# Optimization experiments

Hardware: AMD Instinct MI355X
Metric: run time of the kernel (lower is better)

## Reference

```python
import jax, jax.numpy as jnp
import numpy as np
import math

C_MUL = 32            # multiplicity per irrep
N_NODES = 20000
N_EDGES = 320000
N_RBF = 16
# CG-allowed paths (l_in, l_sh, l_out) with l_in in {0,1}, l_sh,l_out in {0,1,2}
PATHS = [(0,0,0),(0,1,1),(0,2,2),(1,0,1),(1,1,0),(1,1,1),(1,1,2),(1,2,1),(1,2,2)]
DIM_IN = C_MUL * 4
DIM_OUT = C_MUL * 9
N_W = len(PATHS) * C_MUL


def _cg_complex(l1, l2, l3):
    """Clebsch-Gordan coefficients in the complex SH basis (Racah formula)."""
    f = math.factorial
    C = np.zeros((2*l1+1, 2*l2+1, 2*l3+1))
    for m1 in range(-l1, l1+1):
        for m2 in range(-l2, l2+1):
            m3 = m1 + m2
            if abs(m3) > l3:
                continue
            pref = math.sqrt((2*l3+1) * f(l1+l2-l3) * f(l1-l2+l3) * f(-l1+l2+l3) / f(l1+l2+l3+1))
            pref *= math.sqrt(f(l3+m3) * f(l3-m3) * f(l1-m1) * f(l1+m1) * f(l2-m2) * f(l2+m2))
            s = 0.0
            for k in range(0, l1+l2-l3+1):
                args = [k, l1+l2-l3-k, l1-m1-k, l2+m2-k, l3-l2+m1+k, l3-l1-m2+k]
                if min(args) < 0:
                    continue
                d = 1.0
                for a in args:
                    d *= f(a)
                s += (-1.0)**k / d
            C[m1+l1, m2+l2, m3+l3] = pref * s
    return C


def _u_real(l):
    """Complex->real SH change of basis, rows indexed by real m=-l..l."""
    U = np.zeros((2*l+1, 2*l+1), dtype=complex)
    U[l, l] = 1.0
    s = 1.0 / math.sqrt(2.0)
    for m in range(1, l+1):
        U[l+m, l+m] = (-1)**m * s
        U[l+m, l-m] = s
        U[l-m, l-m] = 1j * s
        U[l-m, l+m] = -1j * (-1)**m * s
    return U


def _cg_real(l1, l2, l3):
    """CG coefficients in the real SH basis (real up to a global phase)."""
    Cc = _cg_complex(l1, l2, l3).astype(complex)
    T = np.einsum('am,bn,co,mno->abc', _u_real(l1), _u_real(l2), np.conj(_u_real(l3)), Cc)
    R = T.real if np.abs(T.real).max() >= np.abs(T.imag).max() else T.imag
    return np.ascontiguousarray(R).astype(np.float32)

CGS = [jnp.asarray(_cg_real(*p)) for p in PATHS]


def _sph(v):
    """Real spherical harmonics (l=0,1,2) of unit vectors v: list of (E,1),(E,3),(E,5)."""
    x, y, z = v[:, 0], v[:, 1], v[:, 2]
    s3 = math.sqrt(3.0)
    y0 = jnp.ones_like(x)[:, None]
    y1 = jnp.stack([y, z, x], axis=-1)                       # m = -1, 0, 1
    y2 = jnp.stack([s3*x*y, s3*y*z, 0.5*(3.0*z*z - 1.0), s3*x*z, 0.5*s3*(x*x - y*y)], axis=-1)
    return [y0, y1, y2]


def _tfn_forward(node_features, edge_features, edge_vectors, edge_index, W0, W1, W2):
    E = edge_index.shape[0]
    N = node_features.shape[0]
    # normalized edge vectors -> spherical harmonic basis
    v = edge_vectors / (jnp.linalg.norm(edge_vectors, axis=-1, keepdims=True) + 1e-12)
    Y = _sph(v)
    # radial filter network: Dense->swish x3, bias-free (activation after last layer too)
    h = jax.nn.silu(edge_features @ W0)
    h = jax.nn.silu(h @ W1)
    w = jax.nn.silu(h @ W2)                                  # (E, 9*C)
    # gather source node features and split into irrep blocks
    src = node_features[edge_index[:, 0]]                    # (E, 128)
    xin = [src[:, :C_MUL].reshape(E, C_MUL, 1),              # l=0 block
           src[:, C_MUL:].reshape(E, C_MUL, 3)]              # l=1 block
    outs = [jnp.zeros((E, C_MUL, 2*l+1), node_features.dtype) for l in (0, 1, 2)]
    for p, (l1, l2, l3) in enumerate(PATHS):
        wp = w[:, p*C_MUL:(p+1)*C_MUL]                       # (E, C) per-channel path weight
        contrib = jnp.einsum('abc,eua,eb->euc', CGS[p], xin[l1], Y[l2])
        outs[l3] = outs[l3] + contrib * wp[:, :, None]
    msg = jnp.concatenate([o.reshape(E, -1) for o in outs], axis=-1)   # (E, 288)
    # scatter-add messages to destination nodes
    return jax.ops.segment_sum(msg, edge_index[:, 1], num_segments=N)


def setup_inputs() -> dict:
    key = jax.random.key(0)
    ks = jax.random.split(key, 7)
    node_features = jax.random.normal(ks[0], (N_NODES, DIM_IN), jnp.float32)
    edge_features = jax.random.uniform(ks[1], (N_EDGES, N_RBF), jnp.float32)
    edge_vectors = jax.random.normal(ks[2], (N_EDGES, 3), jnp.float32)
    edge_index = jax.random.randint(ks[3], (N_EDGES, 2), 0, N_NODES, dtype=jnp.int32)
    W0 = jax.random.normal(ks[4], (N_RBF, 64), jnp.float32) * math.sqrt(2.0 / N_RBF)
    W1 = jax.random.normal(ks[5], (64, 64), jnp.float32) * math.sqrt(2.0 / 64)
    W2 = jax.random.normal(ks[6], (64, N_W), jnp.float32) * math.sqrt(2.0 / 64)
    return {"node_features": node_features, "edge_features": edge_features,
            "edge_vectors": edge_vectors, "edge_index": edge_index,
            "W0": W0, "W1": W1, "W2": W2}


def reference(node_features, edge_features, edge_vectors, edge_index, W0, W1, W2):
    return _tfn_forward(node_features, edge_features, edge_vectors, edge_index, W0, W1, W2)
```

## Files before the change

kernel.cpp:

```cpp
#include <hip/hip_runtime.h>
#include <hip/hip_bf16.h>
#include <math.h>

#define TPB 256
#define TE  64
#define HP  72
#define EP  40
#define WP  72
#define CP  90
#define QC  80

#define WBF_USH 26624

typedef float  v4f __attribute__((ext_vector_type(4)));
typedef short  s8v __attribute__((ext_vector_type(8)));
typedef float  f4v __attribute__((ext_vector_type(4)));


__device__ double dfact(int n){ double r = 1.0; for (int i = 2; i <= n; ++i) r *= (double)i; return r; }

__device__ void build_u(int l, double ur[5][5], double ui[5][5]){
  for (int i = 0; i < 5; ++i) for (int j = 0; j < 5; ++j){ ur[i][j] = 0.0; ui[i][j] = 0.0; }
  ur[l][l] = 1.0;
  double s = 1.0 / sqrt(2.0);
  for (int m = 1; m <= l; ++m){
    double sg = (m & 1) ? -1.0 : 1.0;
    ur[l + m][l + m] = sg * s;
    ur[l + m][l - m] = s;
    ui[l - m][l - m] = s;
    ui[l - m][l + m] = -sg * s;
  }
}

__device__ void cg_compute(int tid, float* __restrict__ cg){
  if (tid >= 245) return;
  const int L1[9]  = {0,0,0,1,1,1,1,1,1};
  const int L2[9]  = {0,1,2,0,1,1,1,2,2};
  const int L3[9]  = {0,1,2,1,0,1,2,1,2};
  const int OFF[10] = {0,1,10,35,44,53,80,125,170,245};
  int p = 0;
  while (p < 8 && tid >= OFF[p+1]) ++p;
  int idx = tid - OFF[p];
  int l1 = L1[p], l2 = L2[p], l3 = L3[p];
  int n1 = 2*l1+1, n2 = 2*l2+1, n3 = 2*l3+1;
  int c = idx % n3; int ab = idx / n3; int b = ab % n2; int a = ab / n2;

  double Cc[5][5][5];
  for (int i = 0; i < 5; ++i) for (int j = 0; j < 5; ++j) for (int k = 0; k < 5; ++k) Cc[i][j][k] = 0.0;
  for (int m1 = -l1; m1 <= l1; ++m1) for (int m2 = -l2; m2 <= l2; ++m2){
    int m3 = m1 + m2;
    if (m3 < -l3 || m3 > l3) continue;
    double pref = sqrt((double)(2*l3+1) * dfact(l1+l2-l3) * dfact(l1-l2+l3) * dfact(-l1+l2+l3) / dfact(l1+l2+l3+1));
    pref *= sqrt(dfact(l3+m3)*dfact(l3-m3)*dfact(l1-m1)*dfact(l1+m1)*dfact(l2-m2)*dfact(l2+m2));
    double s = 0.0;
    for (int k = 0; k <= l1 + l2 - l3; ++k){
      int a0 = k, a1 = l1+l2-l3-k, a2 = l1-m1-k, a3 = l2+m2-k, a4 = l3-l2+m1+k, a5 = l3-l1-m2+k;
      if (a0 < 0 || a1 < 0 || a2 < 0 || a3 < 0 || a4 < 0 || a5 < 0) continue;
      double dd = dfact(a0)*dfact(a1)*dfact(a2)*dfact(a3)*dfact(a4)*dfact(a5);
      s += ((k & 1) ? -1.0 : 1.0) / dd;
    }
    Cc[m1+l1][m2+l2][m3+l3] = pref * s;
  }

  double U1r[5][5], U1i[5][5], U2r[5][5], U2i[5][5], U3r[5][5], U3i[5][5];
  build_u(l1, U1r, U1i); build_u(l2, U2r, U2i); build_u(l3, U3r, U3i);

  double sr = 0.0, si = 0.0;
  for (int m = 0; m < n1; ++m) for (int n = 0; n < n2; ++n) for (int o = 0; o < n3; ++o){
    double cc = Cc[m][n][o];
    if (cc == 0.0) continue;
    double xre = U1r[a][m], xim = U1i[a][m];
    double yre = U2r[b][n], yim = U2i[b][n];
    double zr = xre*yre - xim*yim, zi = xre*yim + xim*yre;
    double wr = U3r[c][o], wi = -U3i[c][o];
    double pr = zr*wr - zi*wi, pi = zr*wi + zi*wr;
    sr += pr * cc; si += pi * cc;
  }
  int use_re = (((l1 + l2 + l3) & 1) == 0);
  cg[tid] = (float)(use_re ? sr : si);
}

__global__ void cg_init_kernel(float* __restrict__ cg){
  cg_compute(threadIdx.x, cg);
}


__device__ __forceinline__ float silu_f(float x){
  float t = __expf(-x);
  return x * __builtin_amdgcn_rcpf(1.0f + t);
}

__device__ __forceinline__ ushort f2bf(float x){
  __hip_bfloat16 h = __float2bfloat16(x);
  return *reinterpret_cast<ushort*>(&h);
}

__device__ __forceinline__ float bf2f(ushort u){
  uint v = (uint)u << 16;
  union { uint i; float f; } c; c.i = v;
  return c.f;
}


__global__ void hist_cg_kernel(const int* __restrict__ ei, int* __restrict__ counts,
                               int E, float* __restrict__ cg, int nb,
                               const float* __restrict__ W0, const float* __restrict__ W1,
                               const float* __restrict__ W2, ushort* __restrict__ wbf){
  int b = blockIdx.x;
  if (b >= nb){
    if (b == nb){ cg_compute(threadIdx.x, cg); return; }
    int gid = (b - nb - 1) * TPB + threadIdx.x;
    #pragma unroll 1
    for (int j = 0; j < 13; ++j){
      int idx = j * 2048 + gid;
      if (idx < 2048){
        int col = idx >> 5, k = idx & 31;
        wbf[idx] = (k < 16) ? f2bf(W0[k*64 + col]) : (ushort)0;
      } else if (idx < 6144){
        int t2 = idx - 2048;
        int col = t2 >> 6, k = t2 & 63;
        wbf[idx] = f2bf(W1[k*64 + col]);
      } else {
        int t2 = idx - 6144;
        int qn = t2 / 5120, rem = t2 % 5120;
        int col = rem >> 6, k = rem & 63;
        int p = col >> 3, uu = col & 7;
        wbf[idx] = (p < 9) ? f2bf(W2[k*288 + p*32 + qn*8 + uu]) : (ushort)0;
      }
    }
    return;
  }
  int i = b * TPB + threadIdx.x;
  if (2*i + 1 < E){
    int4 v = ((const int4*)ei)[i];
    atomicAdd(&counts[v.y], 1);
    atomicAdd(&counts[v.w], 1);
  } else if (2*i < E){
    atomicAdd(&counts[ei[4*i + 1]], 1);
  }
}

__global__ void scan_kernel(const int* __restrict__ counts, int* __restrict__ starts,
                            int* __restrict__ cursor, int* __restrict__ nzrank, int N){
  __shared__ int part[1024];
  __shared__ int pnz[1024];
  int t = threadIdx.x;
  int T = (N + 1023) >> 10;
  int base = t * T;
  int s = 0, z = 0;
  for (int i = 0; i < T; ++i){
    int idx = base + i;
    if (idx < N){ int cc = counts[idx]; s += cc; z += (cc > 0); }
  }
  part[t] = s; pnz[t] = z; __syncthreads();
  for (int off = 1; off < 1024; off <<= 1){
    int v = (t >= off) ? part[t - off] : 0;
    int w = (t >= off) ? pnz[t - off] : 0;
    __syncthreads();
    part[t] += v; pnz[t] += w;
    __syncthreads();
  }
  int excl = (t == 0) ? 0 : part[t - 1];
  int enz  = (t == 0) ? 0 : pnz[t - 1];
  for (int i = 0; i < T; ++i){
    int idx = base + i;
    if (idx < N){
      starts[idx] = excl; cursor[idx] = excl; nzrank[idx] = enz;
      int cc = counts[idx];
      excl += cc; enz += (cc > 0);
    }
  }
  if (t == 1023) starts[N] = part[1023];
}

__global__ void perm_kernel(const int* __restrict__ ei, int* __restrict__ cursor,
                            int* __restrict__ perm, int E){
  int i = blockIdx.x * TPB + threadIdx.x;
  if (2*i + 1 < E){
    int4 v = ((const int4*)ei)[i];
    int p0 = atomicAdd(&cursor[v.y], 1); perm[p0] = 2*i;
    int p1 = atomicAdd(&cursor[v.w], 1); perm[p1] = 2*i + 1;
  } else if (2*i < E){
    int pos = atomicAdd(&cursor[ei[4*i + 1]], 1);
    perm[pos] = 2*i;
  }
}


#define DPPF(x, ctrl, rmask) __int_as_float(__builtin_amdgcn_update_dpp(0, __float_as_int(x), ctrl, rmask, 0xF, true))
#define DPPI(x, ctrl, rmask) __builtin_amdgcn_update_dpp(-2, (x), ctrl, rmask, 0xF, false)

#define SEGSUM(v) { \
  v += m1f  * DPPF(v, 0x111, 0xF); \
  v += m2f  * DPPF(v, 0x112, 0xF); \
  v += m4f  * DPPF(v, 0x114, 0xF); \
  v += m8f  * DPPF(v, 0x118, 0xF); \
  v += m15f * DPPF(v, 0x142, 0xA); \
  v += m31f * DPPF(v, 0x143, 0xC); }

template<bool USE_ROWS>
__global__ void __launch_bounds__(TPB, 4) tfn_mfma_kernel(
    const float* __restrict__ nf, const float* __restrict__ ef,
    const float* __restrict__ ev, const int* __restrict__ ei,
    const ushort* __restrict__ wbf, const float* __restrict__ cg,
    const int* __restrict__ perm, const int* __restrict__ nzrank,
    float* __restrict__ rows, float* __restrict__ out, int E)
{
  __shared__ char ldsb[32256];
  ushort* Hs  = (ushort*)(ldsb);
  ushort* W2h = (ushort*)(ldsb + 9216);
  ushort* Cs  = (ushort*)(ldsb + 20736);
  ushort* EFs = (ushort*)(ldsb);
  ushort* W0b = (ushort*)(ldsb + 5120);
  ushort* H0s = (ushort*)(ldsb + 10240);
  ushort* W1b = (ushort*)(ldsb + 19456);

  const int tid  = threadIdx.x;
  const int el   = tid & 63;
  const int wq   = tid >> 6;
  const int lane = el;

  int t = blockIdx.x * TE + el;
  bool valid = (t < E);
  int e = perm[valid ? t : (E - 1)];
  int d = valid ? ei[2*e + 1] : -1;
  int src = ei[2*e];

  float m1f  = (d == DPPI(d, 0x111, 0xF)) ? 1.f : 0.f;
  float m2f  = (d == DPPI(d, 0x112, 0xF)) ? 1.f : 0.f;
  float m4f  = (d == DPPI(d, 0x114, 0xF)) ? 1.f : 0.f;
  float m8f  = (d == DPPI(d, 0x118, 0xF)) ? 1.f : 0.f;
  float m15f = (d == DPPI(d, 0x142, 0xA)) ? 1.f : 0.f;
  float m31f = (d == DPPI(d, 0x143, 0xC)) ? 1.f : 0.f;

  int nd = __shfl_down(d, 1);
  bool tail = valid && ((lane == 63) || (nd != d));

  int ri = 0;
  if (USE_ROWS) ri = (d >= 0 ? nzrank[d] : 0) + (t >> 6);

  const uint* wbu = (const uint*)wbf;

  {
    const v4f efv = *(const v4f*)(ef + (size_t)e * 16 + wq * 4);
    uint p0 = (uint)f2bf(efv.x) | ((uint)f2bf(efv.y) << 16);
    uint p1 = (uint)f2bf(efv.z) | ((uint)f2bf(efv.w) << 16);
    *(uint*)&EFs[el * EP + wq * 4]          = p0;
    *(uint*)&EFs[el * EP + wq * 4 + 2]      = p1;
    *(uint*)&EFs[el * EP + 16 + wq * 4]     = 0u;
    *(uint*)&EFs[el * EP + 16 + wq * 4 + 2] = 0u;
  }
  {
    const uint* g0 = wbu + tid;
    uint* W0w = (uint*)W0b;
    const int bb = (tid >> 4) * 20 + (tid & 15);
    #pragma unroll
    for (int i = 0; i < 4; ++i) W0w[bb + i*320] = g0[i*256];
  }
  {
    const uint* g1 = wbu + 1024 + tid;
    uint* W1w = (uint*)W1b;
    const int b1 = (tid >> 5) * 36 + (tid & 31);
    #pragma unroll
    for (int i = 0; i < 8; ++i) W1w[b1 + i*288] = g1[i*256];
  }
  __syncthreads();

  const int r = lane & 15, q = lane >> 4;
  const int rowbase = wq * 16;

  {
    s8v a = *(const s8v*)&EFs[(rowbase + r) * EP + q * 8];
    #pragma unroll
    for (int tt = 0; tt < 4; ++tt){
      f4v acc = {0.f, 0.f, 0.f, 0.f};
      s8v b = *(const s8v*)&W0b[(tt*16 + r) * EP + q * 8];
      acc = __builtin_amdgcn_mfma_f32_16x16x32_bf16(a, b, acc, 0, 0, 0);
      #pragma unroll
      for (int rr = 0; rr < 4; ++rr)
        H0s[(rowbase + q*4 + rr) * HP + tt*16 + r] = f2bf(silu_f(acc[rr]));
    }
  }
  __syncthreads();

  {
    s8v a0 = *(const s8v*)&H0s[(rowbase + r) * HP + q * 8];
    s8v a1 = *(const s8v*)&H0s[(rowbase + r) * HP + 32 + q * 8];
    #pragma unroll
    for (int tt = 0; tt < 4; ++tt){
      f4v acc = {0.f, 0.f, 0.f, 0.f};
      s8v b0 = *(const s8v*)&W1b[(tt*16 + r) * HP + q * 8];
      s8v b1 = *(const s8v*)&W1b[(tt*16 + r) * HP + 32 + q * 8];
      acc = __builtin_amdgcn_mfma_f32_16x16x32_bf16(a0, b0, acc, 0, 0, 0);
      acc = __builtin_amdgcn_mfma_f32_16x16x32_bf16(a1, b1, acc, 0, 0, 0);
      #pragma unroll
      for (int rr = 0; rr < 4; ++rr)
        Hs[(rowbase + q*4 + rr) * HP + tt*16 + r] = f2bf(silu_f(acc[rr]));
    }
  }
  __syncthreads();

  uint* W2w = (uint*)W2h;
  const int b2 = (tid >> 5) * 36 + (tid & 31);
  {
    const uint* gq = wbu + 3072 + tid;
    #pragma unroll
    for (int m = 0; m < 10; ++m) W2w[b2 + m*288] = gq[m*256];
  }

  float ex = ev[(size_t)e*3+0], eyv = ev[(size_t)e*3+1], ezv = ev[(size_t)e*3+2];
  float ri2 = __builtin_amdgcn_rcpf(sqrtf(ex*ex + eyv*eyv + ezv*ezv) + 1e-12f);
  float X = ex*ri2, Y = eyv*ri2, Z = ezv*ri2;
  const float s3 = 1.7320508075688772f;
  float Y1v[3] = {Y, Z, X};
  float Y2v[5] = {s3*X*Y, s3*Y*Z, 0.5f*(3.f*Z*Z - 1.f), s3*X*Z, 0.5f*s3*(X*X - Y*Y)};

  float B0 = cg[0];
  float B1[3], B2[5], B3[9], B4[3], B5[9], B6[15], B7[9], B8[15];
  #pragma unroll
  for (int c = 0; c < 3; ++c){ float s = 0.f;
    #pragma unroll
    for (int b = 0; b < 3; ++b) s += cg[1 + b*3 + c] * Y1v[b];
    B1[c] = s; }
  #pragma unroll
  for (int c = 0; c < 5; ++c){ float s = 0.f;
    #pragma unroll
    for (int b = 0; b < 5; ++b) s += cg[10 + b*5 + c] * Y2v[b];
    B2[c] = s; }
  #pragma unroll
  for (int i = 0; i < 9; ++i) B3[i] = cg[35 + i];
  #pragma unroll
  for (int a = 0; a < 3; ++a){ float s = 0.f;
    #pragma unroll
    for (int b = 0; b < 3; ++b) s += cg[44 + a*3 + b] * Y1v[b];
    B4[a] = s; }
  #pragma unroll
  for (int a = 0; a < 3; ++a)
    #pragma unroll
    for (int c = 0; c < 3; ++c){ float s = 0.f;
      #pragma unroll
      for (int b = 0; b < 3; ++b) s += cg[53 + (a*3 + b)*3 + c] * Y1v[b];
      B5[a*3 + c] = s; }
  #pragma unroll
  for (int a = 0; a < 3; ++a)
    #pragma unroll
    for (int c = 0; c < 5; ++c){ float s = 0.f;
      #pragma unroll
      for (int b = 0; b < 3; ++b) s += cg[80 + (a*3 + b)*5 + c] * Y1v[b];
      B6[a*5 + c] = s; }
  #pragma unroll
  for (int a = 0; a < 3; ++a)
    #pragma unroll
    for (int c = 0; c < 3; ++c){ float s = 0.f;
      #pragma unroll
      for (int b = 0; b < 5; ++b) s += cg[125 + (a*5 + b)*3 + c] * Y2v[b];
      B7[a*3 + c] = s; }
  #pragma unroll
  for (int a = 0; a < 3; ++a)
    #pragma unroll
    for (int c = 0; c < 5; ++c){ float s = 0.f;
      #pragma unroll
      for (int b = 0; b < 5; ++b) s += cg[170 + (a*5 + b)*5 + c] * Y2v[b];
      B8[a*5 + c] = s; }

  const float* xr = nf + (size_t)src * 128;
  float* dstrow = USE_ROWS ? (rows + (size_t)ri * 288)
                           : (out + (size_t)(d < 0 ? 0 : d) * 288);

  #pragma unroll 1
  for (int h = 0; h < 4; ++h){
    int u0 = h*8 + wq*2;
    float2 x0p = *(const float2*)(xr + u0);
    float2 xq0 = *(const float2*)(xr + 32 + 3*u0);
    float2 xq1 = *(const float2*)(xr + 32 + 3*u0 + 2);
    float2 xq2 = *(const float2*)(xr + 32 + 3*u0 + 4);

    __syncthreads();

    s8v ha0 = *(const s8v*)&Hs[(rowbase + r) * HP + q * 8];
    s8v ha1 = *(const s8v*)&Hs[(rowbase + r) * HP + 32 + q * 8];
    #pragma unroll 1
    for (int tt = 0; tt < 5; ++tt){
      f4v acc4 = {0.f, 0.f, 0.f, 0.f};
      s8v b0 = *(const s8v*)&W2h[(tt*16 + r) * WP + q * 8];
      s8v b1 = *(const s8v*)&W2h[(tt*16 + r) * WP + 32 + q * 8];
      acc4 = __builtin_amdgcn_mfma_f32_16x16x32_bf16(ha0, b0, acc4, 0, 0, 0);
      acc4 = __builtin_amdgcn_mfma_f32_16x16x32_bf16(ha1, b1, acc4, 0, 0, 0);
      #pragma unroll
      for (int rr = 0; rr < 4; ++rr)
        Cs[(rowbase + q*4 + rr) * CP + tt*16 + r] = f2bf(acc4[rr]);
    }

    __syncthreads();

    #pragma unroll
    for (int j = 0; j < 2; ++j){
      int uuq = wq * 2 + j;
      int u   = h * 8 + uuq;

      float wvj[9];
      #pragma unroll
      for (int p = 0; p < 9; ++p) wvj[p] = silu_f(bf2f(Cs[el * CP + p*8 + uuq]));

      float x0 = (j == 0) ? x0p.x : x0p.y;
      float xa = (j == 0) ? xq0.x : xq1.y;
      float xb = (j == 0) ? xq0.y : xq2.x;
      float xc = (j == 0) ? xq1.x : xq2.y;

      float a0 = wvj[0] * (B0 * x0)
               + wvj[4] * (B4[0]*xa + B4[1]*xb + B4[2]*xc);
      float a1[3];
      #pragma unroll
      for (int c = 0; c < 3; ++c)
        a1[c] = wvj[1] * (B1[c] * x0)
              + wvj[3] * (B3[c]*xa + B3[3+c]*xb + B3[6+c]*xc)
              + wvj[5] * (B5[c]*xa + B5[3+c]*xb + B5[6+c]*xc)
              + wvj[7] * (B7[c]*xa + B7[3+c]*xb + B7[6+c]*xc);
      float a2[5];
      #pragma unroll
      for (int c = 0; c < 5; ++c)
        a2[c] = wvj[2] * (B2[c] * x0)
              + wvj[6] * (B6[c]*xa + B6[5+c]*xb + B6[10+c]*xc)
              + wvj[8] * (B8[c]*xa + B8[5+c]*xb + B8[10+c]*xc);

      SEGSUM(a0);
      #pragma unroll
      for (int c = 0; c < 3; ++c) SEGSUM(a1[c]);
      #pragma unroll
      for (int c = 0; c < 5; ++c) SEGSUM(a2[c]);

      if (tail){
        if (USE_ROWS){
          dstrow[u] = a0;
          #pragma unroll
          for (int c = 0; c < 3; ++c) dstrow[32 + 3*u + c] = a1[c];
          #pragma unroll
          for (int c = 0; c < 5; ++c) dstrow[128 + 5*u + c] = a2[c];
        } else {
          unsafeAtomicAdd(&dstrow[u], a0);
          #pragma unroll
          for (int c = 0; c < 3; ++c) unsafeAtomicAdd(&dstrow[32 + 3*u + c], a1[c]);
          #pragma unroll
          for (int c = 0; c < 5; ++c) unsafeAtomicAdd(&dstrow[128 + 5*u + c], a2[c]);
        }
      }
    }

    if (h < 3){
      const uint* gq = wbu + 3072 + (h+1)*2560 + tid;
      #pragma unroll
      for (int m = 0; m < 10; ++m) W2w[b2 + m*288] = gq[m*256];
    }
  }
}

__global__ void combine_kernel(const float* __restrict__ rows,
                               const int* __restrict__ starts,
                               const int* __restrict__ nzrank,
                               float* __restrict__ out, int N)
{
  int g = threadIdx.x >> 6;
  int c = threadIdx.x & 63;
  int d = blockIdx.x * 4 + g;
  if (d >= N) return;
  int s0 = starts[d], s1 = starts[d + 1];
  float a0 = 0.f, a1 = 0.f, a2 = 0.f, a3 = 0.f, a4 = 0.f;
  if (s1 > s0){
    int r0 = nzrank[d] + (s0 >> 6);
    int r1 = nzrank[d] + ((s1 - 1) >> 6);
    for (int r = r0; r <= r1; ++r){
      const float* row = rows + (size_t)r * 288;
      a0 += row[c];
      a1 += row[c + 64];
      a2 += row[c + 128];
      a3 += row[c + 192];
      if (c < 32) a4 += row[c + 256];
    }
  }
  float* o = out + (size_t)d * 288;
  o[c] = a0; o[c + 64] = a1; o[c + 128] = a2; o[c + 192] = a3;
  if (c < 32) o[c + 256] = a4;
}

__global__ void __launch_bounds__(TPB, 2) tfn_atomic_kernel(
    const float* __restrict__ nf, const float* __restrict__ ef,
    const float* __restrict__ ev, const int* __restrict__ ei,
    const float* __restrict__ W0, const float* __restrict__ W1,
    const float* __restrict__ W2, const float* __restrict__ cg,
    float* __restrict__ out, int E)
{
  int e = blockIdx.x * TPB + threadIdx.x;
  if (e >= E) return;

  float f0[16];
  #pragma unroll
  for (int q = 0; q < 16; ++q) f0[q] = ef[(size_t)e*16 + q];
  float h1[64];
  #pragma unroll
  for (int j = 0; j < 64; ++j) h1[j] = 0.f;
  for (int k = 0; k < 64; ++k){
    float a = 0.f;
    #pragma unroll
    for (int q = 0; q < 16; ++q) a += f0[q] * W0[q*64 + k];
    float g = silu_f(a);
    #pragma unroll
    for (int j = 0; j < 64; ++j) h1[j] += g * W1[k*64 + j];
  }
  #pragma unroll
  for (int j = 0; j < 64; ++j) h1[j] = silu_f(h1[j]);

  float ex = ev[(size_t)e*3+0], eyv = ev[(size_t)e*3+1], ezv = ev[(size_t)e*3+2];
  float ri = __builtin_amdgcn_rcpf(sqrtf(ex*ex + eyv*eyv + ezv*ezv) + 1e-12f);
  float X = ex*ri, Y = eyv*ri, Z = ezv*ri;
  const float s3 = 1.7320508075688772f;
  float Y1v[3] = {Y, Z, X};
  float Y2v[5] = {s3*X*Y, s3*Y*Z, 0.5f*(3.f*Z*Z - 1.f), s3*X*Z, 0.5f*s3*(X*X - Y*Y)};

  float B0 = cg[0];
  float B1[3], B2[5], B3[9], B4[3], B5[9], B6[15], B7[9], B8[15];
  #pragma unroll
  for (int c = 0; c < 3; ++c){ float s = 0.f;
    #pragma unroll
    for (int b = 0; b < 3; ++b) s += cg[1 + b*3 + c] * Y1v[b];
    B1[c] = s; }
  #pragma unroll
  for (int c = 0; c < 5; ++c){ float s = 0.f;
    #pragma unroll
    for (int b = 0; b < 5; ++b) s += cg[10 + b*5 + c] * Y2v[b];
    B2[c] = s; }
  #pragma unroll
  for (int i = 0; i < 9; ++i) B3[i] = cg[35 + i];
  #pragma unroll
  for (int a = 0; a < 3; ++a){ float s = 0.f;
    #pragma unroll
    for (int b = 0; b < 3; ++b) s += cg[44 + a*3 + b] * Y1v[b];
    B4[a] = s; }
  #pragma unroll
  for (int a = 0; a < 3; ++a)
    #pragma unroll
    for (int c = 0; c < 3; ++c){ float s = 0.f;
      #pragma unroll
      for (int b = 0; b < 3; ++b) s += cg[53 + (a*3 + b)*3 + c] * Y1v[b];
      B5[a*3 + c] = s; }
  #pragma unroll
  for (int a = 0; a < 3; ++a)
    #pragma unroll
    for (int c = 0; c < 5; ++c){ float s = 0.f;
      #pragma unroll
      for (int b = 0; b < 3; ++b) s += cg[80 + (a*3 + b)*5 + c] * Y1v[b];
      B6[a*5 + c] = s; }
  #pragma unroll
  for (int a = 0; a < 3; ++a)
    #pragma unroll
    for (int c = 0; c < 3; ++c){ float s = 0.f;
      #pragma unroll
      for (int b = 0; b < 5; ++b) s += cg[125 + (a*5 + b)*3 + c] * Y2v[b];
      B7[a*3 + c] = s; }
  #pragma unroll
  for (int a = 0; a < 3; ++a)
    #pragma unroll
    for (int c = 0; c < 5; ++c){ float s = 0.f;
      #pragma unroll
      for (int b = 0; b < 5; ++b) s += cg[170 + (a*5 + b)*5 + c] * Y2v[b];
      B8[a*5 + c] = s; }

  int src = ei[2*e], dst = ei[2*e + 1];
  const float* xr = nf + (size_t)src * 128;
  float* orow = out + (size_t)dst * 288;

  for (int u = 0; u < 32; ++u){
    float wv[9];
    #pragma unroll
    for (int p = 0; p < 9; ++p) wv[p] = 0.f;
    #pragma unroll
    for (int k = 0; k < 64; ++k){
      float hk = h1[k];
      #pragma unroll
      for (int p = 0; p < 9; ++p) wv[p] += hk * W2[k*288 + p*32 + u];
    }
    #pragma unroll
    for (int p = 0; p < 9; ++p) wv[p] = silu_f(wv[p]);

    float x0 = xr[u];
    float xa = xr[32 + 3*u + 0], xb = xr[32 + 3*u + 1], xc = xr[32 + 3*u + 2];

    float a0 = wv[0] * (B0 * x0)
             + wv[4] * (B4[0]*xa + B4[1]*xb + B4[2]*xc);
    float a1[3];
    #pragma unroll
    for (int c = 0; c < 3; ++c)
      a1[c] = wv[1] * (B1[c] * x0)
            + wv[3] * (B3[c]*xa + B3[3+c]*xb + B3[6+c]*xc)
            + wv[5] * (B5[c]*xa + B5[3+c]*xb + B5[6+c]*xc)
            + wv[7] * (B7[c]*xa + B7[3+c]*xb + B7[6+c]*xc);
    float a2[5];
    #pragma unroll
    for (int c = 0; c < 5; ++c)
      a2[c] = wv[2] * (B2[c] * x0)
            + wv[6] * (B6[c]*xa + B6[5+c]*xb + B6[10+c]*xc)
            + wv[8] * (B8[c]*xa + B8[5+c]*xb + B8[10+c]*xc);

    unsafeAtomicAdd(&orow[u], a0);
    #pragma unroll
    for (int c = 0; c < 3; ++c) unsafeAtomicAdd(&orow[32 + 3*u + c], a1[c]);
    #pragma unroll
    for (int c = 0; c < 5; ++c) unsafeAtomicAdd(&orow[128 + 5*u + c], a2[c]);
  }
}

extern "C" void kernel_launch(void* const* d_in, const int* in_sizes, int n_in,
                              void* d_out, int out_size, void* d_ws, size_t ws_size,
                              hipStream_t stream)
{
  const float* nf = (const float*)d_in[0];
  const float* ef = (const float*)d_in[1];
  const float* ev = (const float*)d_in[2];
  const int*   ei = (const int*)  d_in[3];
  const float* W0 = (const float*)d_in[4];
  const float* W1 = (const float*)d_in[5];
  const float* W2 = (const float*)d_in[6];
  float* out = (float*)d_out;

  int E = in_sizes[3] / 2;
  int N = in_sizes[0] / 128;
  int R = E / 64 + N + 64;

  float*  cg     = (float*)d_ws;
  ushort* wbf    = (ushort*)((float*)d_ws + 256);
  int*    counts = (int*)d_ws + 256 + 13312;
  int*    starts = counts + N;
  int*    cursor = starts + N + 1;
  int*    nzrank = cursor + N;
  int*    perm   = nzrank + N;
  size_t base_off = (size_t)256 + 13312 + 4*(size_t)N + 1 + E;
  size_t rows_off = (base_off + 3) & ~(size_t)3;
  float* rows   = (float*)d_ws + rows_off;

  size_t need_csr  = base_off * 4;
  size_t need_rows = (rows_off + (size_t)R * 288) * 4;

  int hb  = (E + TPB - 1) / TPB;
  int hbv = (E/2 + TPB - 1) / TPB;

  if (ws_size >= need_rows){
    hipMemsetAsync(counts, 0, (size_t)N * sizeof(int), stream);
    hist_cg_kernel<<<hbv + 9, TPB, 0, stream>>>(ei, counts, E, cg, hbv, W0, W1, W2, wbf);
    scan_kernel<<<1, 1024, 0, stream>>>(counts, starts, cursor, nzrank, N);
    perm_kernel<<<hbv, TPB, 0, stream>>>(ei, cursor, perm, E);
    tfn_mfma_kernel<true><<<(E + TE - 1) / TE, TPB, 0, stream>>>(
        nf, ef, ev, ei, wbf, cg, perm, nzrank, rows, out, E);
    combine_kernel<<<(N + 3) / 4, TPB, 0, stream>>>(rows, starts, nzrank, out, N);
  } else if (ws_size >= need_csr){
    hipMemsetAsync(d_out, 0, (size_t)out_size * sizeof(float), stream);
    hipMemsetAsync(counts, 0, (size_t)N * sizeof(int), stream);
    hist_cg_kernel<<<hbv + 9, TPB, 0, stream>>>(ei, counts, E, cg, hbv, W0, W1, W2, wbf);
    scan_kernel<<<1, 1024, 0, stream>>>(counts, starts, cursor, nzrank, N);
    perm_kernel<<<hbv, TPB, 0, stream>>>(ei, cursor, perm, E);
    tfn_mfma_kernel<false><<<(E + TE - 1) / TE, TPB, 0, stream>>>(
        nf, ef, ev, ei, wbf, cg, perm, nzrank, rows, out, E);
  } else {
    hipMemsetAsync(d_out, 0, (size_t)out_size * sizeof(float), stream);
    cg_init_kernel<<<1, 256, 0, stream>>>(cg);
    tfn_atomic_kernel<<<hb, TPB, 0, stream>>>(nf, ef, ev, ei, W0, W1, W2, cg, out, E);
  }
}
```

Baseline: 357.3 us.

## Replace DPP segmented reduction with MFMA one-hot segment-sum matrix multiply

Replaces the per-lane DPP segmented scan over edges sharing a destination with a matrix multiply. A one-hot segment-membership matrix in bf16 is multiplied by the messages, which are split into hi/lo bf16 pairs to keep near-fp32 accuracy, on MFMA. Segment heads are found with a ballot and popcount, and results are written per segment from a key table, with row indices now computed per block. This moves the reduction to matrix cores and makes the writes more coalesced, at the cost of extra LDS traffic, two more barriers per h-iteration and a hi/lo split to preserve precision.

```diff
diff --git a/kernel.cpp b/kernel.cpp
--- a/kernel.cpp
+++ b/kernel.cpp
@@ -9,6 +9,7 @@
 #define WP  72
 #define CP  90
 #define QC  80
+#define ATP 136
 
 #define WBF_USH 26624
 
@@ -99,6 +100,13 @@
   uint v = (uint)u << 16;
   union { uint i; float f; } c; c.i = v;
   return c.f;
+}
+
+__device__ __forceinline__ uint packhl(float a){
+  ushort hi = f2bf(a);
+  float res = a - bf2f(hi);
+  ushort lo = f2bf(res);
+  return (uint)hi | ((uint)lo << 16);
 }
 
 
@@ -186,18 +194,6 @@
   }
 }
 
-
-#define DPPF(x, ctrl, rmask) __int_as_float(__builtin_amdgcn_update_dpp(0, __float_as_int(x), ctrl, rmask, 0xF, true))
-#define DPPI(x, ctrl, rmask) __builtin_amdgcn_update_dpp(-2, (x), ctrl, rmask, 0xF, false)
-
-#define SEGSUM(v) { \
-  v += m1f  * DPPF(v, 0x111, 0xF); \
-  v += m2f  * DPPF(v, 0x112, 0xF); \
-  v += m4f  * DPPF(v, 0x114, 0xF); \
-  v += m8f  * DPPF(v, 0x118, 0xF); \
-  v += m15f * DPPF(v, 0x142, 0xA); \
-  v += m31f * DPPF(v, 0x143, 0xC); }
-
 template<bool USE_ROWS>
 __global__ void __launch_bounds__(TPB, 4) tfn_mfma_kernel(
     const float* __restrict__ nf, const float* __restrict__ ef,
@@ -206,7 +202,7 @@
     const int* __restrict__ perm, const int* __restrict__ nzrank,
     float* __restrict__ rows, float* __restrict__ out, int E)
 {
-  __shared__ char ldsb[32256];
+  __shared__ char ldsb[32640];
   ushort* Hs  = (ushort*)(ldsb);
   ushort* W2h = (ushort*)(ldsb + 9216);
   ushort* Cs  = (ushort*)(ldsb + 20736);
@@ -214,6 +210,8 @@
   ushort* W0b = (ushort*)(ldsb + 5120);
   ushort* H0s = (ushort*)(ldsb + 10240);
   ushort* W1b = (ushort*)(ldsb + 19456);
+  ushort* sidtab = (ushort*)(ldsb + 32256);
+  int*    keytab = (int*)(ldsb + 32384);
 
   const int tid  = threadIdx.x;
   const int el   = tid & 63;
@@ -226,18 +224,18 @@
   int d = valid ? ei[2*e + 1] : -1;
   int src = ei[2*e];
 
-  float m1f  = (d == DPPI(d, 0x111, 0xF)) ? 1.f : 0.f;
-  float m2f  = (d == DPPI(d, 0x112, 0xF)) ? 1.f : 0.f;
-  float m4f  = (d == DPPI(d, 0x114, 0xF)) ? 1.f : 0.f;
-  float m8f  = (d == DPPI(d, 0x118, 0xF)) ? 1.f : 0.f;
-  float m15f = (d == DPPI(d, 0x142, 0xA)) ? 1.f : 0.f;
-  float m31f = (d == DPPI(d, 0x143, 0xC)) ? 1.f : 0.f;
-
-  int nd = __shfl_down(d, 1);
-  bool tail = valid && ((lane == 63) || (nd != d));
-
-  int ri = 0;
-  if (USE_ROWS) ri = (d >= 0 ? nzrank[d] : 0) + (t >> 6);
+  int prevd = __shfl_up(d, 1);
+  bool head = (lane == 0) || (d != prevd);
+  unsigned long long hm = __ballot(head);
+  int sid  = __popcll(hm << (63 - lane)) - 1;
+  int nseg = __popcll(hm);
+  sidtab[el] = (ushort)sid;
+  if (head){
+    int key;
+    if (USE_ROWS) key = (d >= 0) ? (nzrank[d] + (int)blockIdx.x) : -1;
+    else          key = d;
+    keytab[sid] = key;
+  }
 
   const uint* wbu = (const uint*)wbf;
 
@@ -269,6 +267,22 @@
   const int r = lane & 15, q = lane >> 4;
   const int rowbase = wq * 16;
 
+  s8v self_[4];
+  {
+    #pragma unroll
+    for (int ks = 0; ks < 4; ++ks){
+      s8v f;
+      #pragma unroll
+      for (int ii = 0; ii < 4; ++ii){
+        int se = sidtab[16*ks + q*4 + ii];
+        short one = (se == wq*16 + r) ? (short)0x3F80 : (short)0;
+        f[2*ii]   = one;
+        f[2*ii+1] = one;
+      }
+      self_[ks] = f;
+    }
+  }
+
   {
     s8v a = *(const s8v*)&EFs[(rowbase + r) * EP + q * 8];
     #pragma unroll
@@ -364,8 +378,6 @@
       B8[a*5 + c] = s; }
 
   const float* xr = nf + (size_t)src * 128;
-  float* dstrow = USE_ROWS ? (rows + (size_t)ri * 288)
-                           : (out + (size_t)(d < 0 ? 0 : d) * 288);
 
   #pragma unroll 1
   for (int h = 0; h < 4; ++h){
@@ -393,10 +405,10 @@
 
     __syncthreads();
 
+    uint pk[2][9];
     #pragma unroll
     for (int j = 0; j < 2; ++j){
       int uuq = wq * 2 + j;
-      int u   = h * 8 + uuq;
 
       float wvj[9];
       #pragma unroll
@@ -409,42 +421,83 @@
 
       float a0 = wvj[0] * (B0 * x0)
                + wvj[4] * (B4[0]*xa + B4[1]*xb + B4[2]*xc);
-      float a1[3];
-      #pragma unroll
-      for (int c = 0; c < 3; ++c)
-        a1[c] = wvj[1] * (B1[c] * x0)
-              + wvj[3] * (B3[c]*xa + B3[3+c]*xb + B3[6+c]*xc)
-              + wvj[5] * (B5[c]*xa + B5[3+c]*xb + B5[6+c]*xc)
-              + wvj[7] * (B7[c]*xa + B7[3+c]*xb + B7[6+c]*xc);
-      float a2[5];
-      #pragma unroll
-      for (int c = 0; c < 5; ++c)
-        a2[c] = wvj[2] * (B2[c] * x0)
-              + wvj[6] * (B6[c]*xa + B6[5+c]*xb + B6[10+c]*xc)
-              + wvj[8] * (B8[c]*xa + B8[5+c]*xb + B8[10+c]*xc);
-
-      SEGSUM(a0);
-      #pragma unroll
-      for (int c = 0; c < 3; ++c) SEGSUM(a1[c]);
-      #pragma unroll
-      for (int c = 0; c < 5; ++c) SEGSUM(a2[c]);
-
-      if (tail){
-        if (USE_ROWS){
-          dstrow[u] = a0;
-          #pragma unroll
-          for (int c = 0; c < 3; ++c) dstrow[32 + 3*u + c] = a1[c];
-          #pragma unroll
-          for (int c = 0; c < 5; ++c) dstrow[128 + 5*u + c] = a2[c];
-        } else {
-          unsafeAtomicAdd(&dstrow[u], a0);
-          #pragma unroll
-          for (int c = 0; c < 3; ++c) unsafeAtomicAdd(&dstrow[32 + 3*u + c], a1[c]);
-          #pragma unroll
-          for (int c = 0; c < 5; ++c) unsafeAtomicAdd(&dstrow[128 + 5*u + c], a2[c]);
+      pk[j][0] = packhl(a0);
+      #pragma unroll
+      for (int c = 0; c < 3; ++c){
+        float a1 = wvj[1] * (B1[c] * x0)
+                 + wvj[3] * (B3[c]*xa + B3[3+c]*xb + B3[6+c]*xc)
+                 + wvj[5] * (B5[c]*xa + B5[3+c]*xb + B5[6+c]*xc)
+                 + wvj[7] * (B7[c]*xa + B7[3+c]*xb + B7[6+c]*xc);
+        pk[j][1+c] = packhl(a1);
+      }
+      #pragma unroll
+      for (int c = 0; c < 5; ++c){
+        float a2 = wvj[2] * (B2[c] * x0)
+                 + wvj[6] * (B6[c]*xa + B6[5+c]*xb + B6[10+c]*xc)
+                 + wvj[8] * (B8[c]*xa + B8[5+c]*xb + B8[10+c]*xc);
+        pk[j][4+c] = packhl(a2);
+      }
+    }
+
+    __syncthreads();
+
+    {
+      uint* AT = (uint*)(ldsb + 9216);
+      #pragma unroll
+      for (int j = 0; j < 2; ++j){
+        int uuq = wq * 2 + j;
+        AT[uuq * (ATP/2) + el] = pk[j][0];
+        #pragma unroll
+        for (int c = 0; c < 3; ++c)
+          AT[(8 + 3*uuq + c) * (ATP/2) + el] = pk[j][1+c];
+        #pragma unroll
+        for (int c = 0; c < 5; ++c)
+          AT[(32 + 5*uuq + c) * (ATP/2) + el] = pk[j][4+c];
+      }
+    }
+
+    __syncthreads();
+
+    {
+      const ushort* ATr = (const ushort*)(ldsb + 9216);
+      f4v racc[5];
+      #pragma unroll
+      for (int tt = 0; tt < 5; ++tt){
+        f4v rc = {0.f, 0.f, 0.f, 0.f};
+        #pragma unroll
+        for (int ks = 0; ks < 4; ++ks){
+          s8v bb = *(const s8v*)&ATr[(tt*16 + r) * ATP + ks*32 + q*8];
+          rc = __builtin_amdgcn_mfma_f32_16x16x32_bf16(self_[ks], bb, rc, 0, 0, 0);
+        }
+        racc[tt] = rc;
+      }
+      #pragma unroll
+      for (int rr = 0; rr < 4; ++rr){
+        int s = wq*16 + q*4 + rr;
+        if (s < nseg){
+          int key = keytab[s];
+          if (key >= 0){
+            float* rp = USE_ROWS ? (rows + (size_t)key * 288)
+                                 : (out  + (size_t)key * 288);
+            #pragma unroll
+            for (int tt = 0; tt < 5; ++tt){
+              int chp = tt*16 + r;
+              if (chp < 72){
+                int g;
+                if (chp < 8)       g = h*8 + chp;
+                else if (chp < 32) g = 32 + 24*h + (chp - 8);
+                else               g = 128 + 40*h + (chp - 32);
+                float v = racc[tt][rr];
+                if (USE_ROWS) rp[g] = v;
+                else          unsafeAtomicAdd(&rp[g], v);
+              }
+            }
+          }
         }
       }
     }
+
+    __syncthreads();
 
     if (h < 3){
       const uint* gq = wbu + 3072 + (h+1)*2560 + tid;
```

Result: slower. 381.6 us (+6.8%).

## Drop per-block row buffer and combine pass; use atomics and packed float2 math

Applied to the files above, without the earlier changes.

Removes the rows-workspace path, in which each 64-edge block wrote partial sums per destination segment and a separate combine kernel reduced them. Segment tails now atomically add straight into the zeroed output. The per-edge tensor-product arithmetic is also rewritten with two-wide float vectors, so the two channels a wave handles can map to packed FMA instructions, and the two bf16 weights are read with one 32-bit LDS load. This saves the rows write/read traffic and a kernel launch, at the cost of global float atomics with contention at segment boundaries and nondeterministic summation order.

```diff
diff --git a/kernel.cpp b/kernel.cpp
--- a/kernel.cpp
+++ b/kernel.cpp
@@ -15,6 +15,7 @@
 typedef float  v4f __attribute__((ext_vector_type(4)));
 typedef short  s8v __attribute__((ext_vector_type(8)));
 typedef float  f4v __attribute__((ext_vector_type(4)));
+typedef float  f2v __attribute__((ext_vector_type(2)));
 
 
 __device__ double dfact(int n){ double r = 1.0; for (int i = 2; i <= n; ++i) r *= (double)i; return r; }
@@ -198,13 +199,11 @@
   v += m15f * DPPF(v, 0x142, 0xA); \
   v += m31f * DPPF(v, 0x143, 0xC); }
 
-template<bool USE_ROWS>
 __global__ void __launch_bounds__(TPB, 4) tfn_mfma_kernel(
     const float* __restrict__ nf, const float* __restrict__ ef,
     const float* __restrict__ ev, const int* __restrict__ ei,
     const ushort* __restrict__ wbf, const float* __restrict__ cg,
-    const int* __restrict__ perm, const int* __restrict__ nzrank,
-    float* __restrict__ rows, float* __restrict__ out, int E)
+    const int* __restrict__ perm, float* __restrict__ out, int E)
 {
   __shared__ char ldsb[32256];
   ushort* Hs  = (ushort*)(ldsb);
@@ -236,9 +235,6 @@
   int nd = __shfl_down(d, 1);
   bool tail = valid && ((lane == 63) || (nd != d));
 
-  int ri = 0;
-  if (USE_ROWS) ri = (d >= 0 ? nzrank[d] : 0) + (t >> 6);
-
   const uint* wbu = (const uint*)wbf;
 
   {
@@ -364,8 +360,7 @@
       B8[a*5 + c] = s; }
 
   const float* xr = nf + (size_t)src * 128;
-  float* dstrow = USE_ROWS ? (rows + (size_t)ri * 288)
-                           : (out + (size_t)(d < 0 ? 0 : d) * 288);
+  float* dstrow = out + (size_t)(d < 0 ? 0 : d) * 288;
 
   #pragma unroll 1
   for (int h = 0; h < 4; ++h){
@@ -393,57 +388,68 @@
 
     __syncthreads();
 
-    #pragma unroll
-    for (int j = 0; j < 2; ++j){
-      int uuq = wq * 2 + j;
-      int u   = h * 8 + uuq;
-
-      float wvj[9];
-      #pragma unroll
-      for (int p = 0; p < 9; ++p) wvj[p] = silu_f(bf2f(Cs[el * CP + p*8 + uuq]));
-
-      float x0 = (j == 0) ? x0p.x : x0p.y;
-      float xa = (j == 0) ? xq0.x : xq1.y;
-      float xb = (j == 0) ? xq0.y : xq2.x;
-      float xc = (j == 0) ? xq1.x : xq2.y;
-
-      float a0 = wvj[0] * (B0 * x0)
-               + wvj[4] * (B4[0]*xa + B4[1]*xb + B4[2]*xc);
-      float a1[3];
+    {
+      f2v wv2[9];
+      #pragma unroll
+      for (int p = 0; p < 9; ++p){
+        uint w = *(const uint*)&Cs[el * CP + p*8 + wq*2];
+        f2v v2; v2.x = silu_f(bf2f((ushort)(w & 0xFFFF)));
+        v2.y = silu_f(bf2f((ushort)(w >> 16)));
+        wv2[p] = v2;
+      }
+
+      f2v x02; x02.x = x0p.x; x02.y = x0p.y;
+      f2v xa2; xa2.x = xq0.x; xa2.y = xq1.y;
+      f2v xb2; xb2.x = xq0.y; xb2.y = xq2.x;
+      f2v xc2; xc2.x = xq1.x; xc2.y = xq2.y;
+
+      f2v a0 = wv2[0] * (B0 * x02)
+             + wv2[4] * (B4[0]*xa2 + B4[1]*xb2 + B4[2]*xc2);
+      f2v a1[3];
       #pragma unroll
       for (int c = 0; c < 3; ++c)
-        a1[c] = wvj[1] * (B1[c] * x0)
-              + wvj[3] * (B3[c]*xa + B3[3+c]*xb + B3[6+c]*xc)
-              + wvj[5] * (B5[c]*xa + B5[3+c]*xb + B5[6+c]*xc)
-              + wvj[7] * (B7[c]*xa + B7[3+c]*xb + B7[6+c]*xc);
-      float a2[5];
+        a1[c] = wv2[1] * (B1[c] * x02)
+              + wv2[3] * (B3[c]*xa2 + B3[3+c]*xb2 + B3[6+c]*xc2)
+              + wv2[5] * (B5[c]*xa2 + B5[3+c]*xb2 + B5[6+c]*xc2)
+              + wv2[7] * (B7[c]*xa2 + B7[3+c]*xb2 + B7[6+c]*xc2);
+      f2v a2[5];
       #pragma unroll
       for (int c = 0; c < 5; ++c)
-        a2[c] = wvj[2] * (B2[c] * x0)
-              + wvj[6] * (B6[c]*xa + B6[5+c]*xb + B6[10+c]*xc)
-              + wvj[8] * (B8[c]*xa + B8[5+c]*xb + B8[10+c]*xc);
-
-      SEGSUM(a0);
-      #pragma unroll
-      for (int c = 0; c < 3; ++c) SEGSUM(a1[c]);
-      #pragma unroll
-      for (int c = 0; c < 5; ++c) SEGSUM(a2[c]);
-
-      if (tail){
-        if (USE_ROWS){
-          dstrow[u] = a0;
-          #pragma unroll
-          for (int c = 0; c < 3; ++c) dstrow[32 + 3*u + c] = a1[c];
-          #pragma unroll
-          for (int c = 0; c < 5; ++c) dstrow[128 + 5*u + c] = a2[c];
-        } else {
-          unsafeAtomicAdd(&dstrow[u], a0);
-          #pragma unroll
-          for (int c = 0; c < 3; ++c) unsafeAtomicAdd(&dstrow[32 + 3*u + c], a1[c]);
-          #pragma unroll
-          for (int c = 0; c < 5; ++c) unsafeAtomicAdd(&dstrow[128 + 5*u + c], a2[c]);
+        a2[c] = wv2[2] * (B2[c] * x02)
+              + wv2[6] * (B6[c]*xa2 + B6[5+c]*xb2 + B6[10+c]*xc2)
+              + wv2[8] * (B8[c]*xa2 + B8[5+c]*xb2 + B8[10+c]*xc2);
+
+      {
+        float v;
+        v = a0.x; SEGSUM(v); a0.x = v;
+        v = a0.y; SEGSUM(v); a0.y = v;
+        #pragma unroll
+        for (int c = 0; c < 3; ++c){
+          v = a1[c].x; SEGSUM(v); a1[c].x = v;
+          v = a1[c].y; SEGSUM(v); a1[c].y = v;
+        }
+        #pragma unroll
+        for (int c = 0; c < 5; ++c){
+          v = a2[c].x; SEGSUM(v); a2[c].x = v;
+          v = a2[c].y; SEGSUM(v); a2[c].y = v;
         }
       }
+
+      if (tail){
+        int u = u0;
+        unsafeAtomicAdd(&dstrow[u],     a0.x);
+        unsafeAtomicAdd(&dstrow[u + 1], a0.y);
+        #pragma unroll
+        for (int c = 0; c < 3; ++c){
+          unsafeAtomicAdd(&dstrow[32 + 3*u + c],     a1[c].x);
+          unsafeAtomicAdd(&dstrow[32 + 3*(u+1) + c], a1[c].y);
+        }
+        #pragma unroll
+        for (int c = 0; c < 5; ++c){
+          unsafeAtomicAdd(&dstrow[128 + 5*u + c],     a2[c].x);
+          unsafeAtomicAdd(&dstrow[128 + 5*(u+1) + c], a2[c].y);
+        }
+      }
     }
 
     if (h < 3){
@@ -452,34 +458,6 @@
       for (int m = 0; m < 10; ++m) W2w[b2 + m*288] = gq[m*256];
     }
   }
-}
-
-__global__ void combine_kernel(const float* __restrict__ rows,
-                               const int* __restrict__ starts,
-                               const int* __restrict__ nzrank,
-                               float* __restrict__ out, int N)
-{
-  int g = threadIdx.x >> 6;
-  int c = threadIdx.x & 63;
-  int d = blockIdx.x * 4 + g;
-  if (d >= N) return;
-  int s0 = starts[d], s1 = starts[d + 1];
-  float a0 = 0.f, a1 = 0.f, a2 = 0.f, a3 = 0.f, a4 = 0.f;
-  if (s1 > s0){
-    int r0 = nzrank[d] + (s0 >> 6);
-    int r1 = nzrank[d] + ((s1 - 1) >> 6);
-    for (int r = r0; r <= r1; ++r){
-      const float* row = rows + (size_t)r * 288;
-      a0 += row[c];
-      a1 += row[c + 64];
-      a2 += row[c + 128];
-      a3 += row[c + 192];
-      if (c < 32) a4 += row[c + 256];
-    }
-  }
-  float* o = out + (size_t)d * 288;
-  o[c] = a0; o[c + 64] = a1; o[c + 128] = a2; o[c + 192] = a3;
-  if (c < 32) o[c + 256] = a4;
 }
 
 __global__ void __launch_bounds__(TPB, 2) tfn_atomic_kernel(
@@ -623,7 +601,6 @@
 
   int E = in_sizes[3] / 2;
   int N = in_sizes[0] / 128;
-  int R = E / 64 + N + 64;
 
   float*  cg     = (float*)d_ws;
   ushort* wbf    = (ushort*)((float*)d_ws + 256);
@@ -633,31 +610,19 @@
   int*    nzrank = cursor + N;
   int*    perm   = nzrank + N;
   size_t base_off = (size_t)256 + 13312 + 4*(size_t)N + 1 + E;
-  size_t rows_off = (base_off + 3) & ~(size_t)3;
-  float* rows   = (float*)d_ws + rows_off;
-
-  size_t need_csr  = base_off * 4;
-  size_t need_rows = (rows_off + (size_t)R * 288) * 4;
+  size_t need_csr = base_off * 4;
 
   int hb  = (E + TPB - 1) / TPB;
   int hbv = (E/2 + TPB - 1) / TPB;
 
-  if (ws_size >= need_rows){
-    hipMemsetAsync(counts, 0, (size_t)N * sizeof(int), stream);
-    hist_cg_kernel<<<hbv + 9, TPB, 0, stream>>>(ei, counts, E, cg, hbv, W0, W1, W2, wbf);
-    scan_kernel<<<1, 1024, 0, stream>>>(counts, starts, cursor, nzrank, N);
-    perm_kernel<<<hbv, TPB, 0, stream>>>(ei, cursor, perm, E);
-    tfn_mfma_kernel<true><<<(E + TE - 1) / TE, TPB, 0, stream>>>(
-        nf, ef, ev, ei, wbf, cg, perm, nzrank, rows, out, E);
-    combine_kernel<<<(N + 3) / 4, TPB, 0, stream>>>(rows, starts, nzrank, out, N);
-  } else if (ws_size >= need_csr){
+  if (ws_size >= need_csr){
     hipMemsetAsync(d_out, 0, (size_t)out_size * sizeof(float), stream);
     hipMemsetAsync(counts, 0, (size_t)N * sizeof(int), stream);
     hist_cg_kernel<<<hbv + 9, TPB, 0, stream>>>(ei, counts, E, cg, hbv, W0, W1, W2, wbf);
     scan_kernel<<<1, 1024, 0, stream>>>(counts, starts, cursor, nzrank, N);
     perm_kernel<<<hbv, TPB, 0, stream>>>(ei, cursor, perm, E);
-    tfn_mfma_kernel<false><<<(E + TE - 1) / TE, TPB, 0, stream>>>(
-        nf, ef, ev, ei, wbf, cg, perm, nzrank, rows, out, E);
+    tfn_mfma_kernel<<<(E + TE - 1) / TE, TPB, 0, stream>>>(
+        nf, ef, ev, ei, wbf, cg, perm, out, E);
   } else {
     hipMemsetAsync(d_out, 0, (size_t)out_size * sizeof(float), stream);
     cg_init_kernel<<<1, 256, 0, stream>>>(cg);
```

Measured after the change: 717.8 us. +100.9%, slower.
